# Performance work log

Measured on AMD Instinct MI355X. Metric: run time of the kernel, lower is better.

## Reference

```python
import jax, jax.numpy as jnp
import numpy as np

NUM_EMBEDDINGS = 1024
EMBEDDING_DIM = 64
COMMITMENT_COST = 0.25
N = 131072


def setup_inputs() -> dict:
    key = jax.random.key(0)
    k1, k2 = jax.random.split(key)
    inputs = jax.random.normal(k1, (N, EMBEDDING_DIM), dtype=jnp.float32)
    # torch init: uniform(-1/num_embeddings, 1/num_embeddings)
    codebook = jax.random.uniform(
        k2, (NUM_EMBEDDINGS, EMBEDDING_DIM), dtype=jnp.float32,
        minval=-1.0 / NUM_EMBEDDINGS, maxval=1.0 / NUM_EMBEDDINGS)
    return {"inputs": inputs, "codebook": codebook}


def reference(inputs, codebook):
    # squared euclidean distances (same argmin as torch.cdist):
    x_sq = jnp.sum(inputs * inputs, axis=1, keepdims=True)            # [N, 1]
    e_sq = jnp.sum(codebook * codebook, axis=1)                       # [K]
    dist2 = x_sq - 2.0 * (inputs @ codebook.T) + e_sq[None, :]        # [N, K]
    encodings_idxs = jnp.argmin(dist2, axis=1)                        # [N]
    quantized = codebook[encodings_idxs]                              # [N, D]

    e_latent_loss = jnp.mean((jax.lax.stop_gradient(quantized) - inputs) ** 2)
    q_latent_loss = jnp.mean((quantized - jax.lax.stop_gradient(inputs)) ** 2)
    vq_loss = q_latent_loss + COMMITMENT_COST * e_latent_loss

    # straight-through estimator
    quantized_st = inputs + jax.lax.stop_gradient(quantized - inputs)

    # perplexity via mean of one-hot == histogram of code usage / N
    counts = jnp.zeros((NUM_EMBEDDINGS,), jnp.float32).at[encodings_idxs].add(1.0)
    avg_probs = counts / inputs.shape[0]
    perplexity = jnp.exp(-jnp.sum(avg_probs * jnp.log(avg_probs + 1e-10)))

    return vq_loss, quantized_st, perplexity
```

## Files before the change

### kernel.cpp

```cpp
#include <hip/hip_runtime.h>
#include <math.h>

#define N_ROWS 131072
#define DIM 64
#define K_CODES 1024
#define CHUNK 256
#define BLK_ROWS 256
#define THREADS 256

typedef __attribute__((ext_vector_type(8))) short bf16x8;
typedef __attribute__((ext_vector_type(4))) float f32x4;

__device__ inline unsigned short bf16_rn(float f) {
    unsigned int u = __builtin_bit_cast(unsigned int, f);
    u += 0x7fffu + ((u >> 16) & 1u);
    return (unsigned short)(u >> 16);
}
__device__ inline float bf16_to_f(unsigned short h) {
    unsigned int u = ((unsigned int)h) << 16;
    return __builtin_bit_cast(float, u);
}


__global__ void vq_prep(const float* __restrict__ cb, float* __restrict__ esq,
                        uint4* __restrict__ cbhi, uint4* __restrict__ cblo) {
    const int k = blockIdx.x * blockDim.x + threadIdx.x;
    if (k >= K_CODES) return;
    const float4* c = (const float4*)(cb + (size_t)k * DIM);
    float s = 0.f;
#pragma unroll
    for (int i = 0; i < 8; ++i) {
        float4 a = c[2 * i], b = c[2 * i + 1];
        float f[8] = {a.x, a.y, a.z, a.w, b.x, b.y, b.z, b.w};
        unsigned int hw[4], lw[4];
#pragma unroll
        for (int p = 0; p < 4; ++p) {
            float f0 = f[2 * p], f1 = f[2 * p + 1];
            s = fmaf(f0, f0, s);
            s = fmaf(f1, f1, s);
            unsigned short h0 = bf16_rn(f0), h1 = bf16_rn(f1);
            unsigned short l0 = bf16_rn(f0 - bf16_to_f(h0));
            unsigned short l1 = bf16_rn(f1 - bf16_to_f(h1));
            hw[p] = (unsigned int)h0 | ((unsigned int)h1 << 16);
            lw[p] = (unsigned int)l0 | ((unsigned int)l1 << 16);
        }
        cbhi[(size_t)k * 8 + i] = make_uint4(hw[0], hw[1], hw[2], hw[3]);
        cblo[(size_t)k * 8 + i] = make_uint4(lw[0], lw[1], lw[2], lw[3]);
    }
    esq[k] = s;
}

__global__ __launch_bounds__(THREADS, 2) void vq_main(
    const float* __restrict__ x, const float* __restrict__ cb,
    const float* __restrict__ esq_g,
    const uint4* __restrict__ cbhi, const uint4* __restrict__ cblo,
    float* __restrict__ outq,
    double* __restrict__ loss_sum, unsigned int* __restrict__ counts)
{
    __shared__ __align__(16) char s_hi[CHUNK * 128];
    __shared__ __align__(16) char s_lo[CHUNK * 128];
    __shared__ __align__(16) float s_esq[K_CODES];
    __shared__ float s_red[THREADS];

    const int t  = threadIdx.x;
    const int w  = t >> 6;
    const int l  = t & 63;
    const int g  = l >> 4;
    const int li = l & 15;

    const int R0 = blockIdx.x * BLK_ROWS;

    bf16x8 xh[4][2], xl[4][2];
#pragma unroll
    for (int rg = 0; rg < 4; ++rg) {
        const int row = R0 + w * 64 + rg * 16 + li;
        const float* xp = x + (size_t)row * DIM;
#pragma unroll
        for (int h = 0; h < 2; ++h) {
            const float4 p0 = *(const float4*)(xp + h * 32 + g * 8);
            const float4 p1 = *(const float4*)(xp + h * 32 + g * 8 + 4);
            float f[8] = {p0.x, p0.y, p0.z, p0.w, p1.x, p1.y, p1.z, p1.w};
            bf16x8 hv, lv;
#pragma unroll
            for (int j = 0; j < 8; ++j) {
                unsigned short hb = bf16_rn(f[j]);
                unsigned short lb = bf16_rn(f[j] - bf16_to_f(hb));
                hv[j] = (short)hb;
                lv[j] = (short)lb;
            }
            xh[rg][h] = hv;
            xl[rg][h] = lv;
        }
    }

    ((float4*)s_esq)[t] = ((const float4*)esq_g)[t];

    float best[4];
    int   bidx[4];
#pragma unroll
    for (int rg = 0; rg < 4; ++rg) { best[rg] = 3.4e38f; bidx[rg] = 0; }

    for (int chunk = 0; chunk < K_CODES / CHUNK; ++chunk) {
        if (chunk) __syncthreads();
#pragma unroll
        for (int i = 0; i < 8; ++i) {
            const int n = i * THREADS + t;
            const int c = n >> 3, s = n & 7;
            const int dst = c * 128 + (((s ^ (c & 7))) << 4);
            *(uint4*)(s_hi + dst) = cbhi[(size_t)(chunk * CHUNK + c) * 8 + s];
            *(uint4*)(s_lo + dst) = cblo[(size_t)(chunk * CHUNK + c) * 8 + s];
        }
        __syncthreads();

#pragma unroll 1
        for (int tb = 0; tb < CHUNK / 16; ++tb) {
            const int c  = tb * 16 + li;
            const int sw = c & 7;
            const int b0 = c * 128 + (((0 + g) ^ sw) << 4);
            const int b1 = c * 128 + (((4 + g) ^ sw) << 4);
            const bf16x8 ah0 = *(const bf16x8*)(s_hi + b0);
            const bf16x8 ah1 = *(const bf16x8*)(s_hi + b1);
            const bf16x8 al0 = *(const bf16x8*)(s_lo + b0);
            const bf16x8 al1 = *(const bf16x8*)(s_lo + b1);
            const int cb0 = chunk * CHUNK + tb * 16 + g * 4;
            const float4 e4 = *(const float4*)(s_esq + cb0);
#pragma unroll
            for (int rg = 0; rg < 4; ++rg) {
                f32x4 acc = {0.f, 0.f, 0.f, 0.f};
                acc = __builtin_amdgcn_mfma_f32_16x16x32_bf16(ah0, xh[rg][0], acc, 0, 0, 0);
                acc = __builtin_amdgcn_mfma_f32_16x16x32_bf16(ah1, xh[rg][1], acc, 0, 0, 0);
                acc = __builtin_amdgcn_mfma_f32_16x16x32_bf16(ah0, xl[rg][0], acc, 0, 0, 0);
                acc = __builtin_amdgcn_mfma_f32_16x16x32_bf16(ah1, xl[rg][1], acc, 0, 0, 0);
                acc = __builtin_amdgcn_mfma_f32_16x16x32_bf16(al0, xh[rg][0], acc, 0, 0, 0);
                acc = __builtin_amdgcn_mfma_f32_16x16x32_bf16(al1, xh[rg][1], acc, 0, 0, 0);
                float t0 = fmaf(-2.f, acc[0], e4.x);
                float t1 = fmaf(-2.f, acc[1], e4.y);
                float t2 = fmaf(-2.f, acc[2], e4.z);
                float t3 = fmaf(-2.f, acc[3], e4.w);
                if (t0 < best[rg]) { best[rg] = t0; bidx[rg] = cb0 + 0; }
                if (t1 < best[rg]) { best[rg] = t1; bidx[rg] = cb0 + 1; }
                if (t2 < best[rg]) { best[rg] = t2; bidx[rg] = cb0 + 2; }
                if (t3 < best[rg]) { best[rg] = t3; bidx[rg] = cb0 + 3; }
            }
        }
    }

#pragma unroll
    for (int rg = 0; rg < 4; ++rg) {
#pragma unroll
        for (int d = 16; d <= 32; d <<= 1) {
            float ob = __shfl_xor(best[rg], d, 64);
            int   oi = __shfl_xor(bidx[rg], d, 64);
            if (ob < best[rg] || (ob == best[rg] && oi < bidx[rg])) {
                best[rg] = ob;
                bidx[rg] = oi;
            }
        }
    }

    float ls = 0.f;
#pragma unroll
    for (int rg = 0; rg < 4; ++rg) {
        const int row = R0 + w * 64 + rg * 16 + li;
        const int idx = bidx[rg];
        if (g == 0) atomicAdd(&counts[idx], 1u);
        const float4* qp = (const float4*)(cb + (size_t)idx * DIM);
        float* op = outq + (size_t)row * DIM;
#pragma unroll
        for (int h = 0; h < 2; ++h) {
            float4 q0 = qp[h * 8 + g * 2];
            float4 q1 = qp[h * 8 + g * 2 + 1];
            *(float4*)(op + h * 32 + g * 8)     = q0;
            *(float4*)(op + h * 32 + g * 8 + 4) = q1;
            float qq[8] = {q0.x, q0.y, q0.z, q0.w, q1.x, q1.y, q1.z, q1.w};
#pragma unroll
            for (int j = 0; j < 8; ++j) {
                float xv = bf16_to_f((unsigned short)xh[rg][h][j])
                         + bf16_to_f((unsigned short)xl[rg][h][j]);
                float e = qq[j] - xv;
                ls = fmaf(e, e, ls);
            }
        }
    }

    s_red[t] = ls;
    __syncthreads();
#pragma unroll
    for (int s = THREADS / 2; s > 0; s >>= 1) {
        if (t < s) s_red[t] += s_red[t + s];
        __syncthreads();
    }
    if (t == 0) atomicAdd(loss_sum, (double)s_red[0]);
}

__global__ void vq_finalize(const unsigned int* __restrict__ counts,
                            const double* __restrict__ loss_sum,
                            float* __restrict__ out) {
    const int t = threadIdx.x;
    float p = (float)counts[t] * (1.0f / (float)N_ROWS);
    float term = p * logf(p + 1e-10f);

    __shared__ float red[1024];
    red[t] = term;
    __syncthreads();
#pragma unroll
    for (int s = 512; s > 0; s >>= 1) {
        if (t < s) red[t] += red[t + s];
        __syncthreads();
    }
    if (t == 0) {
        float H = -red[0];
        double mean = *loss_sum / (double)((size_t)N_ROWS * DIM);
        out[0] = (float)(1.25 * mean);
        out[1 + (size_t)N_ROWS * DIM] = expf(H);
    }
}

extern "C" void kernel_launch(void* const* d_in, const int* in_sizes, int n_in,
                              void* d_out, int out_size, void* d_ws, size_t ws_size,
                              hipStream_t stream) {
    const float* x  = (const float*)d_in[0];
    const float* cb = (const float*)d_in[1];
    float* out = (float*)d_out;
    char* ws = (char*)d_ws;

    double*       loss   = (double*)ws;
    unsigned int* counts = (unsigned int*)(ws + 256);
    float*        esq    = (float*)(ws + 8192);
    uint4*        cbhi   = (uint4*)(ws + 16384);
    uint4*        cblo   = (uint4*)(ws + 16384 + 131072);

    hipMemsetAsync(ws, 0, 4352, stream);
    vq_prep<<<4, 256, 0, stream>>>(cb, esq, cbhi, cblo);
    vq_main<<<N_ROWS / BLK_ROWS, THREADS, 0, stream>>>(x, cb, esq, cbhi, cblo,
                                                       out + 1, loss, counts);
    vq_finalize<<<1, 1024, 0, stream>>>(counts, loss, out);
}
```

Baseline: 177.3 us.

## Software-pipeline MFMA bursts, fold -2 scale and esq into accumulators, fuse finalize

Pre-scales the bf16 hi/lo codebook split by -2 and seeds the MFMA accumulators with the codebook squared norms, so the per-element fma after each dot product goes away. The inner loop becomes double-buffered: LDS fragments for the next 16-code tile load while the current burst runs, and the four row groups' MFMAs are interleaved to hide dependency latency. The memset and finalize kernel are removed: prep zeroes the counters, and the last block to finish (found with an atomic done counter) computes the loss and perplexity. Risks include higher register pressure from two accumulator sets and correctness relying on the last-block fence pattern.

```diff
diff --git a/kernel.cpp b/kernel.cpp
--- a/kernel.cpp
+++ b/kernel.cpp
@@ -7,6 +7,7 @@
 #define CHUNK 256
 #define BLK_ROWS 256
 #define THREADS 256
+#define NBLK (N_ROWS / BLK_ROWS)
 
 typedef __attribute__((ext_vector_type(8))) short bf16x8;
 typedef __attribute__((ext_vector_type(4))) float f32x4;
@@ -23,9 +24,14 @@
 
 
 __global__ void vq_prep(const float* __restrict__ cb, float* __restrict__ esq,
-                        uint4* __restrict__ cbhi, uint4* __restrict__ cblo) {
+                        uint4* __restrict__ cbhi, uint4* __restrict__ cblo,
+                        unsigned int* __restrict__ counts,
+                        unsigned long long* __restrict__ loss,
+                        unsigned int* __restrict__ done) {
     const int k = blockIdx.x * blockDim.x + threadIdx.x;
     if (k >= K_CODES) return;
+    counts[k] = 0u;
+    if (k == 0) { *loss = 0ull; *done = 0u; }
     const float4* c = (const float4*)(cb + (size_t)k * DIM);
     float s = 0.f;
 #pragma unroll
@@ -38,9 +44,10 @@
             float f0 = f[2 * p], f1 = f[2 * p + 1];
             s = fmaf(f0, f0, s);
             s = fmaf(f1, f1, s);
-            unsigned short h0 = bf16_rn(f0), h1 = bf16_rn(f1);
-            unsigned short l0 = bf16_rn(f0 - bf16_to_f(h0));
-            unsigned short l1 = bf16_rn(f1 - bf16_to_f(h1));
+            float m0 = -2.f * f0, m1 = -2.f * f1;
+            unsigned short h0 = bf16_rn(m0), h1 = bf16_rn(m1);
+            unsigned short l0 = bf16_rn(m0 - bf16_to_f(h0));
+            unsigned short l1 = bf16_rn(m1 - bf16_to_f(h1));
             hw[p] = (unsigned int)h0 | ((unsigned int)h1 << 16);
             lw[p] = (unsigned int)l0 | ((unsigned int)l1 << 16);
         }
@@ -49,18 +56,57 @@
     }
     esq[k] = s;
 }
+
+#define LOADF(H0, H1, L0, L1, EV, tb) do {                              \
+    const int _a0 = aoff0 + (tb) * 2048;                                \
+    const int _a1 = aoff1 + (tb) * 2048;                                \
+    H0 = *(const bf16x8*)(s_ab + _a0);                                  \
+    H1 = *(const bf16x8*)(s_ab + _a1);                                  \
+    L0 = *(const bf16x8*)(s_ab + 32768 + _a0);                         \
+    L1 = *(const bf16x8*)(s_ab + 32768 + _a1);                         \
+    EV = *(const float4*)(eb + (tb) * 16);                              \
+} while (0)
+
+#define BURST(H0, H1, L0, L1, EV, ACC) do {                             \
+    _Pragma("unroll") for (int rg = 0; rg < 4; ++rg)                    \
+        ACC[rg] = (f32x4){EV.x, EV.y, EV.z, EV.w};                      \
+    _Pragma("unroll") for (int rg = 0; rg < 4; ++rg)                    \
+        ACC[rg] = __builtin_amdgcn_mfma_f32_16x16x32_bf16(H0, xh[rg][0], ACC[rg], 0, 0, 0); \
+    _Pragma("unroll") for (int rg = 0; rg < 4; ++rg)                    \
+        ACC[rg] = __builtin_amdgcn_mfma_f32_16x16x32_bf16(H1, xh[rg][1], ACC[rg], 0, 0, 0); \
+    _Pragma("unroll") for (int rg = 0; rg < 4; ++rg)                    \
+        ACC[rg] = __builtin_amdgcn_mfma_f32_16x16x32_bf16(H0, xl[rg][0], ACC[rg], 0, 0, 0); \
+    _Pragma("unroll") for (int rg = 0; rg < 4; ++rg)                    \
+        ACC[rg] = __builtin_amdgcn_mfma_f32_16x16x32_bf16(H1, xl[rg][1], ACC[rg], 0, 0, 0); \
+    _Pragma("unroll") for (int rg = 0; rg < 4; ++rg)                    \
+        ACC[rg] = __builtin_amdgcn_mfma_f32_16x16x32_bf16(L0, xh[rg][0], ACC[rg], 0, 0, 0); \
+    _Pragma("unroll") for (int rg = 0; rg < 4; ++rg)                    \
+        ACC[rg] = __builtin_amdgcn_mfma_f32_16x16x32_bf16(L1, xh[rg][1], ACC[rg], 0, 0, 0); \
+} while (0)
+
+#define COMPARE(ACC) do {                                               \
+    _Pragma("unroll") for (int rg = 0; rg < 4; ++rg) {                  \
+        _Pragma("unroll") for (int j = 0; j < 4; ++j) {                 \
+            float _tv = ACC[rg][j];                                     \
+            if (_tv < best[rg]) { best[rg] = _tv; bidx[rg] = kbase + j; } \
+        }                                                               \
+    }                                                                   \
+} while (0)
 
 __global__ __launch_bounds__(THREADS, 2) void vq_main(
     const float* __restrict__ x, const float* __restrict__ cb,
     const float* __restrict__ esq_g,
     const uint4* __restrict__ cbhi, const uint4* __restrict__ cblo,
     float* __restrict__ outq,
-    double* __restrict__ loss_sum, unsigned int* __restrict__ counts)
+    unsigned long long* __restrict__ loss_sum,
+    unsigned int* __restrict__ counts,
+    unsigned int* __restrict__ done,
+    float* __restrict__ out)
 {
-    __shared__ __align__(16) char s_hi[CHUNK * 128];
-    __shared__ __align__(16) char s_lo[CHUNK * 128];
+    __shared__ __align__(16) char s_ab[CHUNK * 256];
     __shared__ __align__(16) float s_esq[K_CODES];
     __shared__ float s_red[THREADS];
+    __shared__ int s_last;
 
     const int t  = threadIdx.x;
     const int w  = t >> 6;
@@ -100,49 +146,44 @@
 #pragma unroll
     for (int rg = 0; rg < 4; ++rg) { best[rg] = 3.4e38f; bidx[rg] = 0; }
 
+    const int sw = li & 7;
+    const int aoff0 = li * 128 + ((g ^ sw) << 4);
+    const int aoff1 = li * 128 + (((4 + g) ^ sw) << 4);
+
     for (int chunk = 0; chunk < K_CODES / CHUNK; ++chunk) {
         if (chunk) __syncthreads();
 #pragma unroll
         for (int i = 0; i < 8; ++i) {
             const int n = i * THREADS + t;
             const int c = n >> 3, s = n & 7;
-            const int dst = c * 128 + (((s ^ (c & 7))) << 4);
-            *(uint4*)(s_hi + dst) = cbhi[(size_t)(chunk * CHUNK + c) * 8 + s];
-            *(uint4*)(s_lo + dst) = cblo[(size_t)(chunk * CHUNK + c) * 8 + s];
+            const int dst = c * 128 + ((s ^ (c & 7)) << 4);
+            *(uint4*)(s_ab + dst)         = cbhi[(size_t)(chunk * CHUNK + c) * 8 + s];
+            *(uint4*)(s_ab + 32768 + dst) = cblo[(size_t)(chunk * CHUNK + c) * 8 + s];
         }
         __syncthreads();
 
+        int kbase = chunk * CHUNK + g * 4;
+        const float* eb = s_esq + chunk * CHUNK + g * 4;
+
+        bf16x8 Ah0, Ah1, Al0, Al1, Bh0, Bh1, Bl0, Bl1;
+        float4 eA, eB;
+        f32x4 accA[4], accB[4];
+
+        LOADF(Ah0, Ah1, Al0, Al1, eA, 0);
+        LOADF(Bh0, Bh1, Bl0, Bl1, eB, 1);
+        BURST(Ah0, Ah1, Al0, Al1, eA, accA);
 #pragma unroll 1
-        for (int tb = 0; tb < CHUNK / 16; ++tb) {
-            const int c  = tb * 16 + li;
-            const int sw = c & 7;
-            const int b0 = c * 128 + (((0 + g) ^ sw) << 4);
-            const int b1 = c * 128 + (((4 + g) ^ sw) << 4);
-            const bf16x8 ah0 = *(const bf16x8*)(s_hi + b0);
-            const bf16x8 ah1 = *(const bf16x8*)(s_hi + b1);
-            const bf16x8 al0 = *(const bf16x8*)(s_lo + b0);
-            const bf16x8 al1 = *(const bf16x8*)(s_lo + b1);
-            const int cb0 = chunk * CHUNK + tb * 16 + g * 4;
-            const float4 e4 = *(const float4*)(s_esq + cb0);
-#pragma unroll
-            for (int rg = 0; rg < 4; ++rg) {
-                f32x4 acc = {0.f, 0.f, 0.f, 0.f};
-                acc = __builtin_amdgcn_mfma_f32_16x16x32_bf16(ah0, xh[rg][0], acc, 0, 0, 0);
-                acc = __builtin_amdgcn_mfma_f32_16x16x32_bf16(ah1, xh[rg][1], acc, 0, 0, 0);
-                acc = __builtin_amdgcn_mfma_f32_16x16x32_bf16(ah0, xl[rg][0], acc, 0, 0, 0);
-                acc = __builtin_amdgcn_mfma_f32_16x16x32_bf16(ah1, xl[rg][1], acc, 0, 0, 0);
-                acc = __builtin_amdgcn_mfma_f32_16x16x32_bf16(al0, xh[rg][0], acc, 0, 0, 0);
-                acc = __builtin_amdgcn_mfma_f32_16x16x32_bf16(al1, xh[rg][1], acc, 0, 0, 0);
-                float t0 = fmaf(-2.f, acc[0], e4.x);
-                float t1 = fmaf(-2.f, acc[1], e4.y);
-                float t2 = fmaf(-2.f, acc[2], e4.z);
-                float t3 = fmaf(-2.f, acc[3], e4.w);
-                if (t0 < best[rg]) { best[rg] = t0; bidx[rg] = cb0 + 0; }
-                if (t1 < best[rg]) { best[rg] = t1; bidx[rg] = cb0 + 1; }
-                if (t2 < best[rg]) { best[rg] = t2; bidx[rg] = cb0 + 2; }
-                if (t3 < best[rg]) { best[rg] = t3; bidx[rg] = cb0 + 3; }
-            }
-        }
+        for (int p = 0; p < 7; ++p) {
+            LOADF(Ah0, Ah1, Al0, Al1, eA, 2 * p + 2);
+            BURST(Bh0, Bh1, Bl0, Bl1, eB, accB);
+            COMPARE(accA); kbase += 16;
+            LOADF(Bh0, Bh1, Bl0, Bl1, eB, 2 * p + 3);
+            BURST(Ah0, Ah1, Al0, Al1, eA, accA);
+            COMPARE(accB); kbase += 16;
+        }
+        BURST(Bh0, Bh1, Bl0, Bl1, eB, accB);
+        COMPARE(accA); kbase += 16;
+        COMPARE(accB); kbase += 16;
     }
 
 #pragma unroll
@@ -190,29 +231,38 @@
         if (t < s) s_red[t] += s_red[t + s];
         __syncthreads();
     }
-    if (t == 0) atomicAdd(loss_sum, (double)s_red[0]);
-}
-
-__global__ void vq_finalize(const unsigned int* __restrict__ counts,
-                            const double* __restrict__ loss_sum,
-                            float* __restrict__ out) {
-    const int t = threadIdx.x;
-    float p = (float)counts[t] * (1.0f / (float)N_ROWS);
-    float term = p * logf(p + 1e-10f);
-
-    __shared__ float red[1024];
-    red[t] = term;
+    if (t == 0) atomicAdd((double*)loss_sum, (double)s_red[0]);
+
+    if (t == 0) {
+        __threadfence();
+        unsigned int prev = __hip_atomic_fetch_add(done, 1u, __ATOMIC_ACQ_REL,
+                                                   __HIP_MEMORY_SCOPE_AGENT);
+        s_last = (prev == (unsigned int)(NBLK - 1));
+    }
     __syncthreads();
-#pragma unroll
-    for (int s = 512; s > 0; s >>= 1) {
-        if (t < s) red[t] += red[t + s];
+    if (s_last) {
+        float part = 0.f;
+#pragma unroll
+        for (int j = 0; j < 4; ++j) {
+            unsigned int c = __hip_atomic_load(&counts[t + j * 256], __ATOMIC_RELAXED,
+                                               __HIP_MEMORY_SCOPE_AGENT);
+            float pr = (float)c * (1.0f / (float)N_ROWS);
+            part += pr * logf(pr + 1e-10f);
+        }
+        s_red[t] = part;
         __syncthreads();
-    }
-    if (t == 0) {
-        float H = -red[0];
-        double mean = *loss_sum / (double)((size_t)N_ROWS * DIM);
-        out[0] = (float)(1.25 * mean);
-        out[1 + (size_t)N_ROWS * DIM] = expf(H);
+#pragma unroll
+        for (int s = THREADS / 2; s > 0; s >>= 1) {
+            if (t < s) s_red[t] += s_red[t + s];
+            __syncthreads();
+        }
+        if (t == 0) {
+            unsigned long long lb = __hip_atomic_load(loss_sum, __ATOMIC_RELAXED,
+                                                      __HIP_MEMORY_SCOPE_AGENT);
+            double ls_d = __builtin_bit_cast(double, lb);
+            out[0] = (float)(1.25 * ls_d / (double)((size_t)N_ROWS * DIM));
+            out[1 + (size_t)N_ROWS * DIM] = expf(-s_red[0]);
+        }
     }
 }
 
@@ -224,15 +274,14 @@
     float* out = (float*)d_out;
     char* ws = (char*)d_ws;
 
-    double*       loss   = (double*)ws;
-    unsigned int* counts = (unsigned int*)(ws + 256);
-    float*        esq    = (float*)(ws + 8192);
-    uint4*        cbhi   = (uint4*)(ws + 16384);
-    uint4*        cblo   = (uint4*)(ws + 16384 + 131072);
-
-    hipMemsetAsync(ws, 0, 4352, stream);
-    vq_prep<<<4, 256, 0, stream>>>(cb, esq, cbhi, cblo);
-    vq_main<<<N_ROWS / BLK_ROWS, THREADS, 0, stream>>>(x, cb, esq, cbhi, cblo,
-                                                       out + 1, loss, counts);
-    vq_finalize<<<1, 1024, 0, stream>>>(counts, loss, out);
-}
+    unsigned long long* loss   = (unsigned long long*)ws;
+    unsigned int*       done   = (unsigned int*)(ws + 128);
+    unsigned int*       counts = (unsigned int*)(ws + 256);
+    float*              esq    = (float*)(ws + 8192);
+    uint4*              cbhi   = (uint4*)(ws + 16384);
+    uint4*              cblo   = (uint4*)(ws + 16384 + 131072);
+
+    vq_prep<<<4, 256, 0, stream>>>(cb, esq, cbhi, cblo, counts, loss, done);
+    vq_main<<<NBLK, THREADS, 0, stream>>>(x, cb, esq, cbhi, cblo,
+                                          out + 1, loss, counts, done, out);
+}
```

Result: slower. 210.9 us (+19.0%).
